# Optimization experiments

Measured on AMD Instinct MI355X. Metric: run time of the kernel, lower is better.

Reference implementation:

```python
import jax, jax.numpy as jnp
import numpy as np

EPS = 1e-5
B, C, N = 2, 256, 65536


def conv1x1(x, W, b):
    # Conv1d with kernel_size=1: (B,Cin,N) x (Cout,Cin) -> (B,Cout,N)
    return jnp.einsum('oc,bcn->bon', W, x) + b[None, :, None]


def instance_norm(x):
    # InstanceNorm1d, affine=False, biased variance over the spatial dim
    m = jnp.mean(x, axis=-1, keepdims=True)
    v = jnp.var(x, axis=-1, keepdims=True)
    return (x - m) * jax.lax.rsqrt(v + EPS)


def mesh_conv(x, gemm, W, b):
    # MeshCNN MeshConv: gather self + 4 one-ring neighbor edges, symmetric fns, (1,5) conv.
    Bb, Cc, E = x.shape
    xp = jnp.concatenate([jnp.zeros((Bb, Cc, 1), x.dtype), x], axis=2)  # pad slot 0 (for -1/missing)
    eid = jnp.broadcast_to(jnp.arange(E, dtype=gemm.dtype)[None, :, None], (Bb, E, 1))
    Gi = jnp.concatenate([eid, gemm], axis=2) + 1                      # (B,E,5), +1 shift for pad row
    xt = xp.transpose(0, 2, 1)                                          # (B,E+1,C)
    f = jax.vmap(lambda xb, gb: xb[gb])(xt, Gi)                         # (B,E,5,C) gather
    f = f.transpose(0, 3, 1, 2)                                         # (B,C,E,5)
    f0, f1, f2, f3, f4 = (f[..., i] for i in range(5))
    g = jnp.stack([f0, f1 + f3, f2 + f4, jnp.abs(f1 - f3), jnp.abs(f2 - f4)], axis=-1)
    # Conv2d(Cin,Cout,(1,5)) over (B,C,E,5) -> (B,Cout,E)
    return jnp.einsum('ock,bcek->boe', W, g) + b[None, :, None]


def setup_inputs() -> dict:
    key = jax.random.key(0)
    ks = jax.random.split(key, 20)
    s = 0.05
    inp = {
        'x_0': jax.random.normal(ks[0], (B, C, N), jnp.float32),
        'x_1': jax.random.normal(ks[1], (B, C, N), jnp.float32),
        'gemm': jax.random.randint(ks[2], (B, N, 4), 0, N, jnp.int32),
        # conv_a / conv_b: C -> C//4
        'Wa': jax.random.normal(ks[3], (C // 4, C), jnp.float32) * s,
        'ba': jax.random.normal(ks[4], (C // 4,), jnp.float32) * s,
        'Wb': jax.random.normal(ks[5], (C // 4, C), jnp.float32) * s,
        'bb': jax.random.normal(ks[6], (C // 4,), jnp.float32) * s,
        # conv_a_local / conv_b_local: C//2 -> C//2
        'Wal': jax.random.normal(ks[7], (C // 2, C // 2), jnp.float32) * s,
        'bal': jax.random.normal(ks[8], (C // 2,), jnp.float32) * s,
        'Wbl': jax.random.normal(ks[9], (C // 2, C // 2), jnp.float32) * s,
        'bbl': jax.random.normal(ks[10], (C // 2,), jnp.float32) * s,
        # MeshConv weights: (Cout, Cin, 5)
        'Wat': jax.random.normal(ks[11], (C // 2, C // 2, 5), jnp.float32) * s,
        'bat': jax.random.normal(ks[12], (C // 2,), jnp.float32) * s,
        'Wbt': jax.random.normal(ks[13], (C // 2, C // 2, 5), jnp.float32) * s,
        'bbt': jax.random.normal(ks[14], (C // 2,), jnp.float32) * s,
        # fuse convs: C -> C
        'Waf': jax.random.normal(ks[15], (C, C), jnp.float32) * s,
        'baf': jax.random.normal(ks[16], (C,), jnp.float32) * s,
        'Wbf': jax.random.normal(ks[17], (C, C), jnp.float32) * s,
        'bbf': jax.random.normal(ks[18], (C,), jnp.float32) * s,
    }
    return inp


def reference(x_0, x_1, gemm, Wa, ba, Wb, bb, Wal, bal, Wbl, bbl,
              Wat, bat, Wbt, bbt, Waf, baf, Wbf, bbf):
    x_a = conv1x1(x_0, Wa, ba)
    x_b = conv1x1(x_1, Wb, bb)
    x_all = jnp.concatenate([x_a, x_b], axis=1)          # (B, C/2, N)
    a_local = conv1x1(x_all, Wal, bal)
    a_tri = mesh_conv(x_all, gemm, Wat, bat)
    x_a_two = jnp.concatenate([a_local, a_tri], axis=1)  # (B, C, N)
    b_local = conv1x1(x_all, Wbl, bbl)
    b_tri = mesh_conv(x_all, gemm, Wbt, bbt)
    x_b_two = jnp.concatenate([b_local, b_tri], axis=1)
    wa = jax.nn.sigmoid(instance_norm(conv1x1(x_a_two, Waf, baf)))
    wb = jax.nn.sigmoid(instance_norm(conv1x1(x_b_two, Wbf, bbf)))
    w = jax.nn.softmax(jnp.stack([wa, wb], axis=1), axis=1)  # (B,2,C,N)
    return x_0 * w[:, 0] + x_1 * w[:, 1]
```

## Files before the change

### kernel.cpp

```cpp
#include <hip/hip_runtime.h>
#include <stdint.h>

#define NEDGE 65536

typedef __attribute__((ext_vector_type(4))) float f32x4;
typedef __attribute__((ext_vector_type(8))) __bf16 bf16x8;

__device__ __forceinline__ uint16_t f2bf(float f) {
  union { float f; uint32_t u; } v; v.f = f;
  uint32_t r = v.u + 0x7FFFu + ((v.u >> 16) & 1u);
  return (uint16_t)(r >> 16);
}
__device__ __forceinline__ float bflo(uint32_t u) {
  union { uint32_t u; float f; } v; v.u = u << 16; return v.f;
}
__device__ __forceinline__ float bfhi(uint32_t u) {
  union { uint32_t u; float f; } v; v.u = u & 0xFFFF0000u; return v.f;
}
__device__ __forceinline__ uint32_t packbf(float lo, float hi) {
  return (uint32_t)f2bf(lo) | ((uint32_t)f2bf(hi) << 16);
}
__device__ __forceinline__ void gload_lds16(const void* g, void* l) {
  __builtin_amdgcn_global_load_lds(
      (__attribute__((address_space(1))) uint32_t*)(uintptr_t)g,
      (__attribute__((address_space(3))) uint32_t*)l, 16, 0, 0);
}
__device__ __forceinline__ float sigm(float z) { return 1.0f / (1.0f + __expf(-z)); }

__global__ void k_compose(const float* __restrict__ Wal, const float* __restrict__ Wbl,
                          const float* __restrict__ Wat, const float* __restrict__ Wbt,
                          const float* __restrict__ Waf, const float* __restrict__ Wbf,
                          uint16_t* __restrict__ Wt) {
  int id = blockIdx.x * 256 + threadIdx.x;
  if (id >= 512 * 640) return;
  int j = id / 640, kk = id % 640;
  const float* Wf = (j < 256) ? Waf : Wbf;
  const float* Wl = (j < 256) ? Wal : Wbl;
  const float* Wr = (j < 256) ? Wat : Wbt;
  int jj = j & 255;
  float acc = 0.f;
  if (kk < 128) {
    int c = kk;
    for (int o = 0; o < 128; ++o) acc += Wl[o * 128 + c] * Wf[jj * 256 + o];
    for (int o = 0; o < 128; ++o) acc += Wr[(o * 128 + c) * 5 + 0] * Wf[jj * 256 + 128 + o];
  } else {
    int blkid = (kk - 128) >> 7;
    int gk = (blkid == 0) ? 1 : (blkid == 1) ? 3 : (blkid == 2) ? 2 : 4;
    int c = (kk - 128) & 127;
    for (int o = 0; o < 128; ++o) acc += Wr[(o * 128 + c) * 5 + gk] * Wf[jj * 256 + 128 + o];
  }
  Wt[j * 640 + kk] = f2bf(acc);
}

__global__ void k_bias(const float* __restrict__ bal, const float* __restrict__ bat,
                       const float* __restrict__ baf, const float* __restrict__ bbl,
                       const float* __restrict__ bbt, const float* __restrict__ bbf,
                       const float* __restrict__ Waf, const float* __restrict__ Wbf,
                       float* __restrict__ biasF) {
  int id = blockIdx.x * 256 + threadIdx.x;
  if (id >= 512) return;
  const float* Wf = (id < 256) ? Waf : Wbf;
  const float* bl = (id < 256) ? bal : bbl;
  const float* bt = (id < 256) ? bat : bbt;
  const float* bsf = (id < 256) ? baf : bbf;
  int jj = id & 255;
  float acc = bsf[jj];
  for (int o = 0; o < 128; ++o) acc += Wf[jj * 256 + o] * bl[o];
  for (int o = 0; o < 128; ++o) acc += Wf[jj * 256 + 128 + o] * bt[o];
  biasF[id] = acc;
}

__global__ void k_wt1(const float* __restrict__ Wa, const float* __restrict__ Wb,
                      uint16_t* __restrict__ W1bf) {
  int id = blockIdx.x * 256 + threadIdx.x;
  if (id >= 2 * 64 * 256) return;
  int side = id >> 14, r = id & 16383;
  W1bf[id] = f2bf(side ? Wb[r] : Wa[r]);
}

__global__ __launch_bounds__(256) void k1_xa(
    const float* __restrict__ x0, const float* __restrict__ x1,
    const uint16_t* __restrict__ W1bf, const float* __restrict__ ba,
    const float* __restrict__ bb, uint16_t* __restrict__ XA) {
  __shared__ __align__(16) uint16_t Bs[64 * 264];
  int t = threadIdx.x;
  int side = blockIdx.y, b = blockIdx.z;
  int n0 = blockIdx.x * 64;
  const float* xin = (side ? x1 : x0) + (size_t)b * 256 * NEDGE;

  {
    const uint16_t* src = W1bf + side * 64 * 256;
#pragma unroll
    for (int i = 0; i < 8; ++i) {
      int chunk = t * 8 + i;
      int j = chunk >> 5, cp = chunk & 31;
      uint4 v = *(const uint4*)(src + j * 256 + cp * 8);
      *(uint4*)&Bs[j * 264 + cp * 8] = v;
    }
  }
  __syncthreads();

  int wv = t >> 6, l = t & 63;
  int m = l & 15, g = l >> 4;
  int nrow = n0 + wv * 16 + m;

  f32x4 acc[4];
  f32x4 zero = {0.f, 0.f, 0.f, 0.f};
#pragma unroll
  for (int cf = 0; cf < 4; ++cf) acc[cf] = zero;

#pragma unroll
  for (int ks = 0; ks < 8; ++ks) {
    const float* xp = xin + (size_t)(ks * 32 + g * 8) * NEDGE + nrow;
    float xv[8];
#pragma unroll
    for (int i = 0; i < 8; ++i) xv[i] = xp[(size_t)i * NEDGE];
    union { bf16x8 v; uint32_t u[4]; } af;
    af.u[0] = packbf(xv[0], xv[1]);
    af.u[1] = packbf(xv[2], xv[3]);
    af.u[2] = packbf(xv[4], xv[5]);
    af.u[3] = packbf(xv[6], xv[7]);
#pragma unroll
    for (int cf = 0; cf < 4; ++cf) {
      bf16x8 bfr = *(const bf16x8*)&Bs[(cf * 16 + m) * 264 + ks * 32 + g * 8];
      acc[cf] = __builtin_amdgcn_mfma_f32_16x16x32_bf16(af.v, bfr, acc[cf], 0, 0, 0);
    }
  }

  const float* bias = side ? bb : ba;
  uint16_t* XAb = XA + (size_t)b * NEDGE * 128;
#pragma unroll
  for (int cf = 0; cf < 4; ++cf) {
    float bv = bias[cf * 16 + m];
#pragma unroll
    for (int q = 0; q < 4; ++q) {
      int row = n0 + wv * 16 + g * 4 + q;
      XAb[(size_t)row * 128 + side * 64 + cf * 16 + m] = f2bf(acc[cf][q] + bv);
    }
  }
}

__device__ __forceinline__ void feat_pair(uint32_t u1, uint32_t u3, uint32_t& s, uint32_t& d) {
  float a1 = bflo(u1), b1 = bfhi(u1), a3 = bflo(u3), b3 = bfhi(u3);
  s = packbf(a1 + a3, b1 + b3);
  d = packbf(fabsf(a1 - a3), fabsf(b1 - b3));
}
__global__ void k2_gather(const uint16_t* __restrict__ XAb, const int* __restrict__ gidx,
                          uint16_t* __restrict__ G) {
  int t = threadIdx.x;
  int wid = t >> 6, lane = t & 63;
  int wbase = (blockIdx.x * 4 + wid) * 16;
  int g = lane >> 4, sl = lane & 15;
  for (int it = 0; it < 4; ++it) {
    int e0 = wbase + it * 4;
    int myidx = 0;
    if (lane < 16) myidx = gidx[(size_t)e0 * 4 + lane];
    int e = e0 + g;
    int i1 = __shfl(myidx, g * 4 + 0);
    int i2 = __shfl(myidx, g * 4 + 1);
    int i3 = __shfl(myidx, g * 4 + 2);
    int i4 = __shfl(myidx, g * 4 + 3);
    uint4 v1 = ((const uint4*)(XAb + (size_t)i1 * 128))[sl];
    uint4 v2 = ((const uint4*)(XAb + (size_t)i2 * 128))[sl];
    uint4 v3 = ((const uint4*)(XAb + (size_t)i3 * 128))[sl];
    uint4 v4 = ((const uint4*)(XAb + (size_t)i4 * 128))[sl];
    uint4 F1, F3, F2, F4;
    feat_pair(v1.x, v3.x, F1.x, F3.x); feat_pair(v1.y, v3.y, F1.y, F3.y);
    feat_pair(v1.z, v3.z, F1.z, F3.z); feat_pair(v1.w, v3.w, F1.w, F3.w);
    feat_pair(v2.x, v4.x, F2.x, F4.x); feat_pair(v2.y, v4.y, F2.y, F4.y);
    feat_pair(v2.z, v4.z, F2.z, F4.z); feat_pair(v2.w, v4.w, F2.w, F4.w);
    uint4* outr = (uint4*)(G + (size_t)e * 512);
    outr[sl] = F1; outr[16 + sl] = F3; outr[32 + sl] = F2; outr[48 + sl] = F4;
  }
}

__global__ __launch_bounds__(256, 2) void k3_gemm(
    const uint16_t* __restrict__ XAb, const uint16_t* __restrict__ G,
    const uint16_t* __restrict__ Wt, const float* __restrict__ biasF,
    uint16_t* __restrict__ Y) {
  __shared__ __align__(16) uint16_t As[128 * 64];
  __shared__ __align__(16) uint16_t Bs[128 * 64];
  int bx = blockIdx.y;
  int by = blockIdx.x;
  int t = threadIdx.x;
  int ebase = bx * 128;
  int jbase = by * 128;
  int wid = t >> 6, lane = t & 63;
  int wr = wid >> 1, wc = wid & 1;
  int m = lane & 15, half = lane >> 4;

  f32x4 acc[4][4];
  f32x4 zero = {0.f, 0.f, 0.f, 0.f};
#pragma unroll
  for (int r = 0; r < 4; ++r)
#pragma unroll
    for (int c = 0; c < 4; ++c) acc[r][c] = zero;

  for (int s = 0; s < 10; ++s) {
    const uint16_t* srcbase; size_t rstride; int koff;
    if (s < 2) { srcbase = XAb; rstride = 128; koff = s * 64; }
    else       { srcbase = G;   rstride = 512; koff = (s - 2) * 64; }
#pragma unroll
    for (int i = 0; i < 4; ++i) {
      int slot = i * 256 + t;
      int r = slot >> 3, c16 = slot & 7;
      gload_lds16(srcbase + (size_t)(ebase + r) * rstride + koff + c16 * 8, &As[slot * 8]);
    }
#pragma unroll
    for (int i = 0; i < 4; ++i) {
      int slot = i * 256 + t;
      int r = slot >> 3, c16 = slot & 7;
      gload_lds16(Wt + (size_t)(jbase + r) * 640 + s * 64 + c16 * 8, &Bs[slot * 8]);
    }
    asm volatile("s_waitcnt vmcnt(0)" ::: "memory");
    __syncthreads();
#pragma unroll
    for (int kit = 0; kit < 2; ++kit) {
      bf16x8 af[4], bf[4];
#pragma unroll
      for (int r = 0; r < 4; ++r) {
        int row = wr * 64 + r * 16 + m;
        af[r] = *(const bf16x8*)&As[row * 64 + kit * 32 + half * 8];
      }
#pragma unroll
      for (int cf = 0; cf < 4; ++cf) {
        int row = wc * 64 + cf * 16 + m;
        bf[cf] = *(const bf16x8*)&Bs[row * 64 + kit * 32 + half * 8];
      }
#pragma unroll
      for (int r = 0; r < 4; ++r)
#pragma unroll
        for (int cf = 0; cf < 4; ++cf)
          acc[r][cf] = __builtin_amdgcn_mfma_f32_16x16x32_bf16(af[r], bf[cf], acc[r][cf], 0, 0, 0);
    }
    __syncthreads();
  }
#pragma unroll
  for (int cf = 0; cf < 4; ++cf) {
    int col = jbase + wc * 64 + cf * 16 + m;
    float bv = biasF[col];
#pragma unroll
    for (int r = 0; r < 4; ++r) {
      int rowb = ebase + wr * 64 + r * 16 + half * 4;
#pragma unroll
      for (int q = 0; q < 4; ++q) {
        float v = acc[r][cf][q] + bv;
        Y[(size_t)(rowb + q) * 512 + col] = f2bf(v);
      }
    }
  }
}

__global__ void k3b1(const uint16_t* __restrict__ Y, float* __restrict__ part) {
  int t = threadIdx.x, ch = blockIdx.x;
  const uint32_t* Y32 = (const uint32_t*)Y;
  float s1a = 0, s2a = 0, s1b = 0, s2b = 0;
  size_t base = (size_t)ch * 128 * 256 + t;
  for (int r = 0; r < 128; ++r) {
    uint32_t v = Y32[base + (size_t)r * 256];
    float x = bflo(v), y = bfhi(v);
    s1a += x; s2a += x * x; s1b += y; s2b += y * y;
  }
  float* p = part + ((size_t)ch * 512 + 2 * t) * 2;
  p[0] = s1a; p[1] = s2a; p[2] = s1b; p[3] = s2b;
}
__global__ void k3b2(const float* __restrict__ part, float* __restrict__ statF) {
  int col = blockIdx.x, t = threadIdx.x;
  float s1 = 0, s2 = 0;
  for (int k = t; k < 512; k += 128) {
    const float* p = part + ((size_t)k * 512 + col) * 2;
    s1 += p[0]; s2 += p[1];
  }
  for (int off = 32; off; off >>= 1) { s1 += __shfl_down(s1, off); s2 += __shfl_down(s2, off); }
  __shared__ float sh[4];
  if ((t & 63) == 0) { sh[(t >> 6) * 2] = s1; sh[(t >> 6) * 2 + 1] = s2; }
  __syncthreads();
  if (t == 0) {
    s1 = sh[0] + sh[2]; s2 = sh[1] + sh[3];
    float mean = s1 * (1.0f / 65536.0f);
    float var = s2 * (1.0f / 65536.0f) - mean * mean;
    statF[col * 2] = mean;
    statF[col * 2 + 1] = rsqrtf(var + 1e-5f);
  }
}

__global__ __launch_bounds__(256) void k4_final(
    const uint16_t* __restrict__ Y, const float* __restrict__ statF,
    const float* __restrict__ x0b, const float* __restrict__ x1b,
    float* __restrict__ outb) {
  __shared__ float W0[128][65];
  __shared__ float mA[128], rA[128], mB[128], rB[128];
  int t = threadIdx.x;
  int n0 = blockIdx.x * 64;
  int ch = blockIdx.y;
  if (t < 128) {
    mA[t] = statF[(ch * 128 + t) * 2];
    rA[t] = statF[(ch * 128 + t) * 2 + 1];
  } else {
    int q = t - 128;
    mB[q] = statF[(256 + ch * 128 + q) * 2];
    rB[q] = statF[(256 + ch * 128 + q) * 2 + 1];
  }
  __syncthreads();
  const char* Ybase = (const char*)Y;
  for (int i = t; i < 64 * 64; i += 256) {
    int row = i >> 6, cp = i & 63;
    const char* yr = Ybase + (size_t)(n0 + row) * 1024;
    uint32_t ya2 = *(const uint32_t*)(yr + ch * 256 + cp * 4);
    uint32_t yb2 = *(const uint32_t*)(yr + 512 + ch * 256 + cp * 4);
    int c0 = 2 * cp, c1 = 2 * cp + 1;
    float wa0 = sigm((bflo(ya2) - mA[c0]) * rA[c0]);
    float wa1 = sigm((bfhi(ya2) - mA[c1]) * rA[c1]);
    float wb0 = sigm((bflo(yb2) - mB[c0]) * rB[c0]);
    float wb1 = sigm((bfhi(yb2) - mB[c1]) * rB[c1]);
    W0[c0][row] = sigm(wa0 - wb0);
    W0[c1][row] = sigm(wa1 - wb1);
  }
  __syncthreads();
  int nn = t & 63, cg = t >> 6;
  for (int cc = cg; cc < 128; cc += 4) {
    int c = ch * 128 + cc;
    size_t gi = (size_t)c * NEDGE + n0 + nn;
    float w0 = W0[cc][nn];
    outb[gi] = x0b[gi] * w0 + x1b[gi] * (1.0f - w0);
  }
}

extern "C" void kernel_launch(void* const* d_in, const int* in_sizes, int n_in,
                              void* d_out, int out_size, void* d_ws, size_t ws_size,
                              hipStream_t stream) {
  const float* x0 = (const float*)d_in[0];
  const float* x1 = (const float*)d_in[1];
  const int* gemm = (const int*)d_in[2];
  const float* Wa = (const float*)d_in[3];
  const float* ba = (const float*)d_in[4];
  const float* Wb = (const float*)d_in[5];
  const float* bb = (const float*)d_in[6];
  const float* Wal = (const float*)d_in[7];
  const float* bal = (const float*)d_in[8];
  const float* Wbl = (const float*)d_in[9];
  const float* bbl = (const float*)d_in[10];
  const float* Wat = (const float*)d_in[11];
  const float* bat = (const float*)d_in[12];
  const float* Wbt = (const float*)d_in[13];
  const float* bbt = (const float*)d_in[14];
  const float* Waf = (const float*)d_in[15];
  const float* baf = (const float*)d_in[16];
  const float* Wbf = (const float*)d_in[17];
  const float* bbf = (const float*)d_in[18];
  float* out = (float*)d_out;

  char* ws = (char*)d_ws;
  uint16_t* XA   = (uint16_t*)ws;
  uint16_t* G    = (uint16_t*)(ws + 33554432);
  uint16_t* Yb   = (uint16_t*)(ws + 100663296);
  uint16_t* Wt   = (uint16_t*)(ws + 167772160);
  uint16_t* W1bf = (uint16_t*)(ws + 168427520);
  float*    biasF= (float*)(ws + 168558592);
  float*    part = (float*)(ws + 168560640);
  float*    statF= (float*)(ws + 170657792);

  k_compose<<<dim3(1280), dim3(256), 0, stream>>>(Wal, Wbl, Wat, Wbt, Waf, Wbf, Wt);
  k_bias<<<dim3(2), dim3(256), 0, stream>>>(bal, bat, baf, bbl, bbt, bbf, Waf, Wbf, biasF);
  k_wt1<<<dim3(128), dim3(256), 0, stream>>>(Wa, Wb, W1bf);
  k1_xa<<<dim3(1024, 2, 2), dim3(256), 0, stream>>>(x0, x1, W1bf, ba, bb, XA);

  for (int b = 0; b < 2; ++b) {
    const uint16_t* XAb = XA + (size_t)b * NEDGE * 128;
    k2_gather<<<dim3(1024), dim3(256), 0, stream>>>(XAb, gemm + (size_t)b * NEDGE * 4, G);
    k3_gemm<<<dim3(4, 512), dim3(256), 0, stream>>>(XAb, G, Wt, biasF, Yb);
    k3b1<<<dim3(512), dim3(256), 0, stream>>>(Yb, part);
    k3b2<<<dim3(512), dim3(128), 0, stream>>>(part, statF + b * 1024);
    k4_final<<<dim3(1024, 2), dim3(256), 0, stream>>>(
        Yb, statF + b * 1024, x0 + (size_t)b * 256 * NEDGE,
        x1 + (size_t)b * 256 * NEDGE, out + (size_t)b * 256 * NEDGE);
  }
}
```

Measured before the change: 450.5 us.

## Stage k1 input tiles through LDS with double-buffered async loads

The first 1x1-conv kernel now streams x tiles (32 channels by 128 edges) into LDS through async global_load_lds, double-buffered so the next channel slice loads while the MFMAs run on the current one. Weights also go to LDS via async loads with an XOR swizzle in place of padding, and each block covers 128 edges (two row fragments), which halves the grid. This replaces strided per-thread scalar global loads with wide coalesced 16-byte transfers. The cost is more LDS, two barriers per k-step and manual vmcnt waits.

```diff
diff --git a/kernel.cpp b/kernel.cpp
--- a/kernel.cpp
+++ b/kernel.cpp
@@ -82,62 +82,94 @@
     const float* __restrict__ x0, const float* __restrict__ x1,
     const uint16_t* __restrict__ W1bf, const float* __restrict__ ba,
     const float* __restrict__ bb, uint16_t* __restrict__ XA) {
-  __shared__ __align__(16) uint16_t Bs[64 * 264];
+  __shared__ __align__(16) float Xs[2][32 * 128];
+  __shared__ __align__(16) uint16_t Bs[64 * 256];
   int t = threadIdx.x;
   int side = blockIdx.y, b = blockIdx.z;
-  int n0 = blockIdx.x * 64;
-  const float* xin = (side ? x1 : x0) + (size_t)b * 256 * NEDGE;
-
-  {
-    const uint16_t* src = W1bf + side * 64 * 256;
-#pragma unroll
-    for (int i = 0; i < 8; ++i) {
-      int chunk = t * 8 + i;
-      int j = chunk >> 5, cp = chunk & 31;
-      uint4 v = *(const uint4*)(src + j * 256 + cp * 8);
-      *(uint4*)&Bs[j * 264 + cp * 8] = v;
-    }
-  }
-  __syncthreads();
+  int n0 = blockIdx.x * 128;
+  const float* xin = (side ? x1 : x0) + (size_t)b * 256 * NEDGE + n0;
+  const uint16_t* wsrc = W1bf + side * 64 * 256;
+
+#pragma unroll
+  for (int q = 0; q < 8; ++q) {
+    int s = q * 256 + t;
+    int j = s >> 5, pb = s & 31;
+    int lb = pb ^ (j & 7);
+    gload_lds16(wsrc + j * 256 + lb * 8, &Bs[s * 8]);
+  }
+#pragma unroll
+  for (int q = 0; q < 4; ++q) {
+    int s = q * 256 + t;
+    int cl = s >> 5, pb = s & 31;
+    int lb = pb ^ (((cl >> 3) & 3) << 2);
+    gload_lds16(xin + (size_t)cl * NEDGE + lb * 4, &Xs[0][s * 4]);
+  }
 
   int wv = t >> 6, l = t & 63;
   int m = l & 15, g = l >> 4;
-  int nrow = n0 + wv * 16 + m;
-
-  f32x4 acc[4];
+
+  f32x4 acc[2][4];
   f32x4 zero = {0.f, 0.f, 0.f, 0.f};
 #pragma unroll
-  for (int cf = 0; cf < 4; ++cf) acc[cf] = zero;
-
-#pragma unroll
+  for (int rf = 0; rf < 2; ++rf)
+#pragma unroll
+    for (int cf = 0; cf < 4; ++cf) acc[rf][cf] = zero;
+
   for (int ks = 0; ks < 8; ++ks) {
-    const float* xp = xin + (size_t)(ks * 32 + g * 8) * NEDGE + nrow;
-    float xv[8];
-#pragma unroll
-    for (int i = 0; i < 8; ++i) xv[i] = xp[(size_t)i * NEDGE];
-    union { bf16x8 v; uint32_t u[4]; } af;
-    af.u[0] = packbf(xv[0], xv[1]);
-    af.u[1] = packbf(xv[2], xv[3]);
-    af.u[2] = packbf(xv[4], xv[5]);
-    af.u[3] = packbf(xv[6], xv[7]);
+    if (ks < 7) {
+      const float* xc = xin + (size_t)(ks + 1) * 32 * NEDGE;
+#pragma unroll
+      for (int q = 0; q < 4; ++q) {
+        int s = q * 256 + t;
+        int cl = s >> 5, pb = s & 31;
+        int lb = pb ^ (((cl >> 3) & 3) << 2);
+        gload_lds16(xc + (size_t)cl * NEDGE + lb * 4, &Xs[(ks + 1) & 1][s * 4]);
+      }
+      asm volatile("s_waitcnt vmcnt(4)" ::: "memory");
+    } else {
+      asm volatile("s_waitcnt vmcnt(0)" ::: "memory");
+    }
+    __syncthreads();
+
+    const float* Xb = Xs[ks & 1];
+    bf16x8 bfr[4];
 #pragma unroll
     for (int cf = 0; cf < 4; ++cf) {
-      bf16x8 bfr = *(const bf16x8*)&Bs[(cf * 16 + m) * 264 + ks * 32 + g * 8];
-      acc[cf] = __builtin_amdgcn_mfma_f32_16x16x32_bf16(af.v, bfr, acc[cf], 0, 0, 0);
-    }
+      int jloc = cf * 16 + m;
+      int pbb = (ks * 4 + g) ^ (jloc & 7);
+      bfr[cf] = *(const bf16x8*)&Bs[jloc * 256 + pbb * 8];
+    }
+#pragma unroll
+    for (int rf = 0; rf < 2; ++rf) {
+      int nloc = rf * 64 + wv * 16 + m;
+      int phys = (nloc >> 2) ^ (g << 2);
+      const float* base = Xb + phys * 4 + (nloc & 3);
+      float xv[8];
+#pragma unroll
+      for (int i = 0; i < 8; ++i) xv[i] = base[(g * 8 + i) * 128];
+      union { bf16x8 v; __bf16 e[8]; } af;
+#pragma unroll
+      for (int i = 0; i < 8; ++i) af.e[i] = (__bf16)xv[i];
+#pragma unroll
+      for (int cf = 0; cf < 4; ++cf)
+        acc[rf][cf] = __builtin_amdgcn_mfma_f32_16x16x32_bf16(af.v, bfr[cf], acc[rf][cf], 0, 0, 0);
+    }
+    __syncthreads();
   }
 
   const float* bias = side ? bb : ba;
-  uint16_t* XAb = XA + (size_t)b * NEDGE * 128;
-#pragma unroll
-  for (int cf = 0; cf < 4; ++cf) {
-    float bv = bias[cf * 16 + m];
-#pragma unroll
-    for (int q = 0; q < 4; ++q) {
-      int row = n0 + wv * 16 + g * 4 + q;
-      XAb[(size_t)row * 128 + side * 64 + cf * 16 + m] = f2bf(acc[cf][q] + bv);
-    }
-  }
+  uint16_t* XAb = XA + ((size_t)b * NEDGE + n0) * 128 + side * 64;
+#pragma unroll
+  for (int rf = 0; rf < 2; ++rf)
+#pragma unroll
+    for (int cf = 0; cf < 4; ++cf) {
+      float bv = bias[cf * 16 + m];
+#pragma unroll
+      for (int q = 0; q < 4; ++q) {
+        int row = rf * 64 + wv * 16 + g * 4 + q;
+        XAb[(size_t)row * 128 + cf * 16 + m] = f2bf(acc[rf][cf][q] + bv);
+      }
+    }
 }
 
 __device__ __forceinline__ void feat_pair(uint32_t u1, uint32_t u3, uint32_t& s, uint32_t& d) {
@@ -363,7 +395,7 @@
   k_compose<<<dim3(1280), dim3(256), 0, stream>>>(Wal, Wbl, Wat, Wbt, Waf, Wbf, Wt);
   k_bias<<<dim3(2), dim3(256), 0, stream>>>(bal, bat, baf, bbl, bbt, bbf, Waf, Wbf, biasF);
   k_wt1<<<dim3(128), dim3(256), 0, stream>>>(Wa, Wb, W1bf);
-  k1_xa<<<dim3(1024, 2, 2), dim3(256), 0, stream>>>(x0, x1, W1bf, ba, bb, XA);
+  k1_xa<<<dim3(512, 2, 2), dim3(256), 0, stream>>>(x0, x1, W1bf, ba, bb, XA);
 
   for (int b = 0; b < 2; ++b) {
     const uint16_t* XAb = XA + (size_t)b * NEDGE * 128;
```

Result: faster. 434.8 us (-3.5%).
